# Kernel tuning notes

Hardware: AMD Instinct MI355X
Metric: run time of the kernel (lower is better)

## Reference

```python
import jax, jax.numpy as jnp
import numpy as np

N_SERIES = 1024
N_TIME = 600
INPUT_SIZE = 168
OUTPUT_SIZE = 24
N_S = 4
SEAS = 24  # single seasonality period


def setup_inputs() -> dict:
    key = jax.random.key(0)
    k1, k2, k3 = jax.random.split(key, 3)
    # strictly positive series (Holt-Winters multiplicative form divides and logs)
    y = jax.random.uniform(k1, (N_SERIES, N_TIME), jnp.float32) + 0.5
    s_matrix = jax.random.normal(k2, (N_SERIES, N_S), jnp.float32)
    embeds = jax.random.uniform(k3, (N_SERIES, 1 + 1 + SEAS), jnp.float32)
    idxs = jnp.arange(N_SERIES, dtype=jnp.int32)
    return {"y": y, "s_matrix": s_matrix, "embeds": embeds, "idxs": idxs}


def _compute_levels_seasons(y, embeds_rows):
    # embeds_rows: (N, 26) = [lev_sms_logit, seas_sms_logit, 24 log init seasons]
    lev_sms = jax.nn.sigmoid(embeds_rows[:, 0])           # (N,)
    seas_sms = jax.nn.sigmoid(embeds_rows[:, 1])          # (N,)
    init_seas = jnp.exp(embeds_rows[:, 2:2 + SEAS])       # (N, P)

    level0 = y[:, 0] / init_seas[:, 0]                    # (N,)
    # buffer holds seasonalities1[t .. t+P-1]; before step t=1 that is
    # [init[1], ..., init[P-1], init[0]]
    buf0 = jnp.roll(init_seas, -1, axis=1)                # (N, P)

    def step(carry, y_t):
        lev_prev, buf = carry
        s_t = buf[:, 0]
        newlev = lev_sms * (y_t / s_t) + (1.0 - lev_sms) * lev_prev
        news = seas_sms * (y_t / newlev) + (1.0 - seas_sms) * s_t
        buf = jnp.concatenate([buf[:, 1:], news[:, None]], axis=1)
        return (newlev, buf), (newlev, news)

    (_, _), (levs, seas_new) = jax.lax.scan(step, (level0, buf0), y[:, 1:].T)
    levels = jnp.concatenate([level0[:, None], levs.T], axis=1)          # (N, T)
    # seasonalities1 indices 0..P are [init[0..P-1], init[0]], then one new per step
    seas_head = jnp.concatenate([init_seas, init_seas[:, :1]], axis=1)   # (N, P+1)
    seasonalities1 = jnp.concatenate([seas_head, seas_new.T], axis=1)    # (N, T+P)
    return levels, seasonalities1


def reference(y, s_matrix, embeds, idxs):
    embeds_rows = embeds[idxs]                                 # (N, 26)
    levels, seasonalities1 = _compute_levels_seasons(y, embeds_rows)

    n_series, n_time = y.shape
    n_windows = n_time - INPUT_SIZE - OUTPUT_SIZE + 1          # 409
    w = jnp.arange(n_windows)
    idx_in = w[:, None] + jnp.arange(INPUT_SIZE)               # (W, I)
    idx_out = w[:, None] + INPUT_SIZE + jnp.arange(OUTPUT_SIZE)  # (W, O)

    y_in = y[:, idx_in]                                        # (N, W, I)
    lev_end = levels[:, w + INPUT_SIZE - 1]                    # (N, W)
    seas_in = seasonalities1[:, idx_in]                        # (N, W, I)
    y_in_norm = jnp.log(y_in / (lev_end[:, :, None] * seas_in))
    insample = jnp.transpose(y_in_norm, (1, 0, 2))             # (W, N, I)
    static = jnp.broadcast_to(s_matrix[None], (n_windows, n_series, s_matrix.shape[1]))
    windows_y_insample = jnp.concatenate([insample, static], axis=2)  # (W, N, I+n_s)

    # eval mode: outsample windows are raw (un-normalized) targets
    windows_y_outsample = jnp.transpose(y[:, idx_out], (1, 0, 2))     # (W, N, O)

    return (windows_y_insample, windows_y_outsample, levels, seasonalities1)
```

## Files before the change

kernel.cpp:

```cpp
#include <hip/hip_runtime.h>

#define N_SERIES 1024
#define N_TIME 600
#define INPUT_SIZE 168
#define OUTPUT_SIZE 24
#define N_S 4
#define SEAS 24
#define N_WINDOWS (N_TIME - INPUT_SIZE - OUTPUT_SIZE + 1)
#define SEAS_LEN (N_TIME + SEAS)

#define INS_ELEMS (N_WINDOWS * N_SERIES * (INPUT_SIZE + N_S))
#define OUTS_ELEMS (N_WINDOWS * N_SERIES * OUTPUT_SIZE)
#define LEV_ELEMS (N_SERIES * N_TIME)
#define SEAS_ELEMS (N_SERIES * SEAS_LEN)

#define NQ_OUTS (OUTS_ELEMS / 4)

#define SCAN_BLOCKS 16
#define SCAN_T 64
#define COPY_BLOCKS 2032
#define WS_NEEDED (2u * LEV_ELEMS * sizeof(float))

#define INS2_BLOCKS 512
#define SGRP 2
#define TASKS_PER_W (SGRP * 43)
#define TASKS_PER_G (N_WINDOWS * TASKS_PER_W)

typedef float f4 __attribute__((ext_vector_type(4)));

#define WAVE_FENCE()                                   \
    do {                                               \
        __builtin_amdgcn_wave_barrier();               \
        asm volatile("" ::: "memory");                 \
    } while (0)

__global__ __launch_bounds__(SCAN_T) void scan_copy_kernel(
    const float* __restrict__ y, const float* __restrict__ embeds,
    const int* __restrict__ idxs, float* __restrict__ levels,
    float* __restrict__ seas1, f4* __restrict__ out_outs)
{
    __shared__ float b_lev[SCAN_T][25];
    __shared__ float b_sea[SCAN_T][25];

    if (blockIdx.x < SCAN_BLOCKS) {
        const int lane = threadIdx.x;
        const int s0 = blockIdx.x * SCAN_T;
        const int s = s0 + lane;
        const int row = idxs[s];
        const float* e = embeds + row * (2 + SEAS);

        const float lev_sms = 1.0f / (1.0f + __expf(-e[0]));
        const float seas_sms = 1.0f / (1.0f + __expf(-e[1]));
        const float one_m_lev = 1.0f - lev_sms;
        const float one_m_seas = 1.0f - seas_sms;

        const float* yrow = y + s * N_TIME;
        const f4* yv4 = (const f4*)yrow;

        f4 cur[6], nxt[6];
#pragma unroll
        for (int i = 0; i < 6; ++i) cur[i] = yv4[i];

        float sb[SEAS];
#pragma unroll
        for (int j = 0; j < SEAS; ++j) {
            float v = __expf(e[2 + j]);
            sb[j] = v;
            b_sea[lane][j] = v;
        }
        WAVE_FENCE();
#pragma unroll
        for (int k4 = 0; k4 < 6; ++k4) {
            int q4 = lane + k4 * SCAN_T;
            int r = q4 / 6;
            int c4 = q4 - r * 6;
            int cc = c4 * 4;
            f4 v = {b_sea[r][cc], b_sea[r][cc + 1], b_sea[r][cc + 2],
                    b_sea[r][cc + 3]};
            *(f4*)(seas1 + (s0 + r) * SEAS_LEN + cc) = v;
        }
        seas1[s * SEAS_LEN + SEAS] = sb[0];
        float lev = __fdividef(cur[0].x, sb[0]);
        levels[s * N_TIME] = lev;
        WAVE_FENCE();

        {
#pragma unroll
            for (int i = 0; i < 6; ++i) nxt[i] = yv4[6 + i];
#pragma unroll
            for (int j = 0; j < 23; ++j) {
                const int t = j + 1;
                float yt = cur[t >> 2][t & 3];
                float st = sb[t];
                float q1 = __fdividef(yt, st);
                float newlev = lev_sms * q1 + one_m_lev * lev;
                float news =
                    seas_sms * __fdividef(yt, newlev) + one_m_seas * st;
                lev = newlev;
                sb[t] = news;
                b_lev[lane][j] = newlev;
                b_sea[lane][j] = news;
            }
            WAVE_FENCE();
#pragma unroll
            for (int k = 0; k < 24; ++k) {
                int i = lane + k * SCAN_T;
                int r = i / 24;
                int col = i - r * 24;
                if (col < 23) {
                    int sr = s0 + r;
                    levels[sr * N_TIME + 1 + col] = b_lev[r][col];
                    seas1[sr * SEAS_LEN + 25 + col] = b_sea[r][col];
                }
            }
            WAVE_FENCE();
#pragma unroll
            for (int i = 0; i < 6; ++i) cur[i] = nxt[i];
        }

#pragma unroll 1
        for (int c = 1; c < 25; ++c) {
            const int t0 = 24 * c;
            if (c < 24) {
                const f4* p = (const f4*)(yrow + 24 * (c + 1));
#pragma unroll
                for (int i = 0; i < 6; ++i) nxt[i] = p[i];
            }
#pragma unroll
            for (int j = 0; j < 24; ++j) {
                float yt = cur[j >> 2][j & 3];
                float st = sb[j];
                float q1 = __fdividef(yt, st);
                float newlev = lev_sms * q1 + one_m_lev * lev;
                float news =
                    seas_sms * __fdividef(yt, newlev) + one_m_seas * st;
                lev = newlev;
                sb[j] = news;
                b_lev[lane][j] = newlev;
                b_sea[lane][j] = news;
            }
            WAVE_FENCE();
#pragma unroll
            for (int k4 = 0; k4 < 6; ++k4) {
                int q4 = lane + k4 * SCAN_T;
                int r = q4 / 6;
                int c4 = q4 - r * 6;
                int sr = s0 + r;
                int cc = c4 * 4;
                f4 vl = {b_lev[r][cc], b_lev[r][cc + 1], b_lev[r][cc + 2],
                         b_lev[r][cc + 3]};
                *(f4*)(levels + sr * N_TIME + t0 + cc) = vl;
                f4 vs = {b_sea[r][cc], b_sea[r][cc + 1], b_sea[r][cc + 2],
                         b_sea[r][cc + 3]};
                *(f4*)(seas1 + sr * SEAS_LEN + SEAS + t0 + cc) = vs;
            }
            WAVE_FENCE();
#pragma unroll
            for (int i = 0; i < 6; ++i) cur[i] = nxt[i];
        }
    } else {
        int idx = (blockIdx.x - SCAN_BLOCKS) * SCAN_T + threadIdx.x;
        const int stride = (gridDim.x - SCAN_BLOCKS) * SCAN_T;
        for (; idx < NQ_OUTS; idx += stride) {
            int rowq = idx / 6;
            int j4 = idx - rowq * 6;
            int w = rowq >> 10;
            int s = rowq & 1023;
            const float* yp = y + s * N_TIME + w + INPUT_SIZE + j4 * 4;
            f4 v = {yp[0], yp[1], yp[2], yp[3]};
            __builtin_nontemporal_store(v, &out_outs[idx]);
        }
    }
}

__global__ __launch_bounds__(256) void logpass_kernel(
    const float* __restrict__ y, const float* __restrict__ levels,
    const float* __restrict__ seas1, float* __restrict__ tbl,
    float* __restrict__ llv)
{
    int i = blockIdx.x * 256 + threadIdx.x;
    int sr = i / 150;
    int c = i - sr * 150;
    f4 a = *((const f4*)(y + sr * N_TIME) + c);
    f4 se = *((const f4*)(seas1 + sr * SEAS_LEN) + c);
    f4 l = *((const f4*)(levels + sr * N_TIME) + c);
    f4 ta, tl;
    ta.x = __logf(__fdividef(a.x, se.x));
    ta.y = __logf(__fdividef(a.y, se.y));
    ta.z = __logf(__fdividef(a.z, se.z));
    ta.w = __logf(__fdividef(a.w, se.w));
    tl.x = __logf(l.x);
    tl.y = __logf(l.y);
    tl.z = __logf(l.z);
    tl.w = __logf(l.w);
    ((f4*)tbl)[i] = ta;
    ((f4*)llv)[i] = tl;
}

__global__ __launch_bounds__(256) void ins2_kernel(
    const float* __restrict__ tbl, const float* __restrict__ llv,
    const float* __restrict__ y, const float* __restrict__ levels,
    const float* __restrict__ seas1, const float* __restrict__ s_matrix,
    f4* __restrict__ out_ins, int have_ws)
{
    const int s0 = blockIdx.x * SGRP;
    for (int ql = threadIdx.x; ql < TASKS_PER_G; ql += 256) {
        int w = ql / TASKS_PER_W;
        int slot = ql - w * TASKS_PER_W;
        int sl = slot / 43;
        int e4 = slot - sl * 43;
        int s = s0 + sl;
        f4 v;
        if (e4 == 42) {
            v = *(const f4*)(s_matrix + s * N_S);
        } else if (have_ws) {
            int t = w + e4 * 4;
            const float* tp = tbl + s * N_TIME + t;
            float lv = llv[s * N_TIME + w + INPUT_SIZE - 1];
            v.x = tp[0] - lv;
            v.y = tp[1] - lv;
            v.z = tp[2] - lv;
            v.w = tp[3] - lv;
        } else {
            int t = w + e4 * 4;
            float lev = levels[s * N_TIME + w + INPUT_SIZE - 1];
            const float* yp = y + s * N_TIME + t;
            const float* sp = seas1 + s * SEAS_LEN + t;
            v.x = __logf(__fdividef(yp[0], lev * sp[0]));
            v.y = __logf(__fdividef(yp[1], lev * sp[1]));
            v.z = __logf(__fdividef(yp[2], lev * sp[2]));
            v.w = __logf(__fdividef(yp[3], lev * sp[3]));
        }
        __builtin_nontemporal_store(v, &out_ins[w * 44032 + s * 43 + e4]);
    }
}

extern "C" void kernel_launch(void* const* d_in, const int* in_sizes, int n_in,
                              void* d_out, int out_size, void* d_ws, size_t ws_size,
                              hipStream_t stream) {
    const float* y      = (const float*)d_in[0];
    const float* sm     = (const float*)d_in[1];
    const float* embeds = (const float*)d_in[2];
    const int*   idxs   = (const int*)d_in[3];

    float* out      = (float*)d_out;
    float* out_ins  = out;
    float* out_outs = out + INS_ELEMS;
    float* out_lev  = out + INS_ELEMS + OUTS_ELEMS;
    float* out_seas = out_lev + LEV_ELEMS;

    float* tbl = (float*)d_ws;
    float* llv = tbl + LEV_ELEMS;
    const int have_ws = (ws_size >= (size_t)WS_NEEDED) ? 1 : 0;

    scan_copy_kernel<<<SCAN_BLOCKS + COPY_BLOCKS, SCAN_T, 0, stream>>>(
        y, embeds, idxs, out_lev, out_seas, (f4*)out_outs);
    if (have_ws) {
        logpass_kernel<<<LEV_ELEMS / 4 / 256, 256, 0, stream>>>(
            y, out_lev, out_seas, tbl, llv);
    }
    ins2_kernel<<<INS2_BLOCKS, 256, 0, stream>>>(
        tbl, llv, y, out_lev, out_seas, sm, (f4*)out_ins, have_ws);
}
```

Baseline: 127.4 us.

## Fuse log-table pass into insample kernel using shared-memory staging

Removes the separate logpass kernel and workspace tables. Each block now computes log(y/seas) and log(level) for four series into shared memory, stored phase-split by t mod 4 so unaligned window reads stay cheap, and then writes all insample windows from LDS. This cuts one launch and the global round-trip of the intermediate tables. The cost is fewer blocks (256 with 512 threads), which lowers parallelism for a store-bound output.

```diff
diff --git a/kernel.cpp b/kernel.cpp
--- a/kernel.cpp
+++ b/kernel.cpp
@@ -19,12 +19,11 @@
 #define SCAN_BLOCKS 16
 #define SCAN_T 64
 #define COPY_BLOCKS 2032
-#define WS_NEEDED (2u * LEV_ELEMS * sizeof(float))
-
-#define INS2_BLOCKS 512
-#define SGRP 2
-#define TASKS_PER_W (SGRP * 43)
-#define TASKS_PER_G (N_WINDOWS * TASKS_PER_W)
+
+#define INS3_BLOCKS 256
+#define INS3_T 512
+#define TASKS_PER_W 172
+#define TASKS_TOTAL (N_WINDOWS * TASKS_PER_W)
 
 typedef float f4 __attribute__((ext_vector_type(4)));
 
@@ -173,65 +172,54 @@
     }
 }
 
-__global__ __launch_bounds__(256) void logpass_kernel(
-    const float* __restrict__ y, const float* __restrict__ levels,
-    const float* __restrict__ seas1, float* __restrict__ tbl,
-    float* __restrict__ llv)
-{
-    int i = blockIdx.x * 256 + threadIdx.x;
-    int sr = i / 150;
-    int c = i - sr * 150;
-    f4 a = *((const f4*)(y + sr * N_TIME) + c);
-    f4 se = *((const f4*)(seas1 + sr * SEAS_LEN) + c);
-    f4 l = *((const f4*)(levels + sr * N_TIME) + c);
-    f4 ta, tl;
-    ta.x = __logf(__fdividef(a.x, se.x));
-    ta.y = __logf(__fdividef(a.y, se.y));
-    ta.z = __logf(__fdividef(a.z, se.z));
-    ta.w = __logf(__fdividef(a.w, se.w));
-    tl.x = __logf(l.x);
-    tl.y = __logf(l.y);
-    tl.z = __logf(l.z);
-    tl.w = __logf(l.w);
-    ((f4*)tbl)[i] = ta;
-    ((f4*)llv)[i] = tl;
-}
-
-__global__ __launch_bounds__(256) void ins2_kernel(
-    const float* __restrict__ tbl, const float* __restrict__ llv,
+__global__ __launch_bounds__(INS3_T) void ins3_kernel(
     const float* __restrict__ y, const float* __restrict__ levels,
     const float* __restrict__ seas1, const float* __restrict__ s_matrix,
-    f4* __restrict__ out_ins, int have_ws)
+    f4* __restrict__ out_ins)
 {
-    const int s0 = blockIdx.x * SGRP;
-    for (int ql = threadIdx.x; ql < TASKS_PER_G; ql += 256) {
-        int w = ql / TASKS_PER_W;
-        int slot = ql - w * TASKS_PER_W;
-        int sl = slot / 43;
+    __shared__ float tq[4][4][152];
+    __shared__ float lv[4][608];
+    __shared__ f4 sml[4];
+
+    const int tid = threadIdx.x;
+    const int s0 = blockIdx.x * 4;
+
+    for (int i = tid; i < 600; i += INS3_T) {
+        int sl = i / 150;
+        int c = i - sl * 150;
+        int s = s0 + sl;
+        f4 yv = *((const f4*)(y + s * N_TIME) + c);
+        f4 sv = *((const f4*)(seas1 + s * SEAS_LEN) + c);
+        f4 lvv = *((const f4*)(levels + s * N_TIME) + c);
+        tq[sl][0][c] = __logf(__fdividef(yv.x, sv.x));
+        tq[sl][1][c] = __logf(__fdividef(yv.y, sv.y));
+        tq[sl][2][c] = __logf(__fdividef(yv.z, sv.z));
+        tq[sl][3][c] = __logf(__fdividef(yv.w, sv.w));
+        f4 lg = {__logf(lvv.x), __logf(lvv.y), __logf(lvv.z), __logf(lvv.w)};
+        *(f4*)(&lv[sl][4 * c]) = lg;
+    }
+    if (tid < 4) sml[tid] = *((const f4*)s_matrix + (s0 + tid));
+    __syncthreads();
+
+    for (int ql = tid; ql < TASKS_TOTAL; ql += INS3_T) {
+        unsigned uql = (unsigned)ql;
+        int w = uql / 172u;
+        int slot = ql - w * 172;
+        int sl = (unsigned)slot / 43u;
         int e4 = slot - sl * 43;
-        int s = s0 + sl;
         f4 v;
         if (e4 == 42) {
-            v = *(const f4*)(s_matrix + s * N_S);
-        } else if (have_ws) {
-            int t = w + e4 * 4;
-            const float* tp = tbl + s * N_TIME + t;
-            float lv = llv[s * N_TIME + w + INPUT_SIZE - 1];
-            v.x = tp[0] - lv;
-            v.y = tp[1] - lv;
-            v.z = tp[2] - lv;
-            v.w = tp[3] - lv;
+            v = sml[sl];
         } else {
-            int t = w + e4 * 4;
-            float lev = levels[s * N_TIME + w + INPUT_SIZE - 1];
-            const float* yp = y + s * N_TIME + t;
-            const float* sp = seas1 + s * SEAS_LEN + t;
-            v.x = __logf(__fdividef(yp[0], lev * sp[0]));
-            v.y = __logf(__fdividef(yp[1], lev * sp[1]));
-            v.z = __logf(__fdividef(yp[2], lev * sp[2]));
-            v.w = __logf(__fdividef(yp[3], lev * sp[3]));
-        }
-        __builtin_nontemporal_store(v, &out_ins[w * 44032 + s * 43 + e4]);
+            float l = lv[sl][w + INPUT_SIZE - 1];
+            int a0 = w, a1 = w + 1, a2 = w + 2, a3 = w + 3;
+            v.x = tq[sl][a0 & 3][(a0 >> 2) + e4] - l;
+            v.y = tq[sl][a1 & 3][(a1 >> 2) + e4] - l;
+            v.z = tq[sl][a2 & 3][(a2 >> 2) + e4] - l;
+            v.w = tq[sl][a3 & 3][(a3 >> 2) + e4] - l;
+        }
+        __builtin_nontemporal_store(
+            v, &out_ins[w * (N_SERIES * 43) + (s0 + sl) * 43 + e4]);
     }
 }
 
@@ -249,16 +237,10 @@
     float* out_lev  = out + INS_ELEMS + OUTS_ELEMS;
     float* out_seas = out_lev + LEV_ELEMS;
 
-    float* tbl = (float*)d_ws;
-    float* llv = tbl + LEV_ELEMS;
-    const int have_ws = (ws_size >= (size_t)WS_NEEDED) ? 1 : 0;
+    (void)d_ws; (void)ws_size;
 
     scan_copy_kernel<<<SCAN_BLOCKS + COPY_BLOCKS, SCAN_T, 0, stream>>>(
         y, embeds, idxs, out_lev, out_seas, (f4*)out_outs);
-    if (have_ws) {
-        logpass_kernel<<<LEV_ELEMS / 4 / 256, 256, 0, stream>>>(
-            y, out_lev, out_seas, tbl, llv);
-    }
-    ins2_kernel<<<INS2_BLOCKS, 256, 0, stream>>>(
-        tbl, llv, y, out_lev, out_seas, sm, (f4*)out_ins, have_ws);
+    ins3_kernel<<<INS3_BLOCKS, INS3_T, 0, stream>>>(
+        y, out_lev, out_seas, sm, (f4*)out_ins);
 }
```

Result: faster. 112.5 us (-11.7%).
